# Optimization experiments

Measured on AMD Instinct MI355X. Metric: run time of the kernel, lower is better.

Reference implementation:

```python
import jax, jax.numpy as jnp
import numpy as np

# 2nd-order Sobel kernels (kornia get_sobel_kernel2d_2nd_order): d2/dx2, d2/dxdy, d2/dy2
_KXX = np.array([[1., -2., 1.], [2., -4., 2.], [1., -2., 1.]], np.float32)
_KXY = np.array([[-1., 0., 1.], [0., 0., 0.], [1., 0., -1.]], np.float32)
_KERNELS = jnp.asarray(np.stack([_KXX, _KXY, _KXX.T])[:, None])  # (3,1,3,3)


def setup_inputs() -> dict:
    key = jax.random.key(0)
    x = jax.random.normal(key, (16, 3, 1024, 1024), dtype=jnp.float32)
    return {"x": x}


def reference(x):
    scale = 1.0
    B, C, H, W = x.shape
    # spatial_gradient_2nd_order: replicate pad + 3x3 conv per channel
    xp = jnp.pad(x.reshape(B * C, 1, H, W), ((0, 0), (0, 0), (1, 1), (1, 1)), mode='edge')
    g = jax.lax.conv_general_dilated(xp, _KERNELS, (1, 1), 'VALID')  # (B*C, 3, H, W)
    gxx, gxy, gyy = g[:, 0], g[:, 1], g[:, 2]
    # abs determinant of Hessian, clamp
    scores = jnp.abs(gxx * gyy - gxy * gxy) * (scale ** 4)
    scores = jnp.maximum(scores, 1e-6).reshape(B, C, H, W)
    # NMS via 3x3 max-pool (stride 1, SAME): keep only local maxima
    pooled = jax.lax.reduce_window(scores, -jnp.inf, jax.lax.max,
                                   (1, 1, 3, 3), (1, 1, 1, 1), 'SAME')
    scores = jnp.where(scores == pooled, scores, jnp.zeros((), scores.dtype))
    # global max normalization (adaptive_max_pool2d to 1x1)
    smax = jnp.max(scores, axis=(2, 3), keepdims=True)  # (B,C,1,1)
    return scores / smax
```

## Files before the change

### kernel.cpp

```cpp
#include <hip/hip_runtime.h>

#define H 1024
#define W 1024
#define HW (H * W)
#define STRIP 32
#define SLOTF 1024
#define RING 6

typedef __attribute__((address_space(3))) float lds_f;
typedef const __attribute__((address_space(1))) float g_f;
typedef float nfloat4 __attribute__((ext_vector_type(4)));

__device__ __forceinline__ void gload16(const float* g, float* l) {
    __builtin_amdgcn_global_load_lds((g_f*)g, (lds_f*)l, 16, 0, 0);
}

template<int N>
__device__ __forceinline__ void wait_vm_barrier() {
    asm volatile("s_waitcnt vmcnt(%0)\n\ts_barrier" :: "i"(N) : "memory");
}
__device__ __forceinline__ void barrier_only() {
    asm volatile("s_barrier" ::: "memory");
}

__device__ __forceinline__ void stage(const float* px, int row, float* slotbase, int wq, int t) {
    row = row < 0 ? 0 : (row > H - 1 ? H - 1 : row);
    gload16(px + (size_t)row * W + (t << 2), slotbase + wq);
}

__device__ __forceinline__ float score_ref(
    float a00, float a01, float a02,
    float a10, float a11, float a12,
    float a20, float a21, float a22)
{
#pragma clang fp contract(off)
    float gxx = fmaf(-2.0f, a01, a00);
    gxx = gxx + a02;
    gxx = fmaf(2.0f, a10, gxx);
    gxx = fmaf(-4.0f, a11, gxx);
    gxx = fmaf(2.0f, a12, gxx);
    gxx = gxx + a20;
    gxx = fmaf(-2.0f, a21, gxx);
    gxx = gxx + a22;
    float gxy = a02 - a00;
    gxy = gxy + a20;
    gxy = gxy - a22;
    float gyy = fmaf(2.0f, a01, a00);
    gyy = gyy + a02;
    gyy = fmaf(-2.0f, a10, gyy);
    gyy = fmaf(-4.0f, a11, gyy);
    gyy = fmaf(-2.0f, a12, gyy);
    gyy = gyy + a20;
    gyy = fmaf(2.0f, a21, gyy);
    gyy = gyy + a22;

    float p1 = gxx * gyy;
    float p2 = gxy * gxy;
    float det = p1 - p2;
    float s = fabsf(det);
    return s > 1e-6f ? s : 1e-6f;
}

struct Row8 { float a[8]; };

__device__ __forceinline__ Row8 read_win(const float* p, int t)
{
    const int c = t << 2;
    const float2 L  = *(const float2*)(p + (t == 0 ? 0 : c - 2));
    const float4 M  = *(const float4*)(p + c);
    const float2 Rr = *(const float2*)(p + (t == 255 ? 1022 : c + 4));
    Row8 r;
    r.a[0] = L.x;
    r.a[1] = (t == 0) ? L.x : L.y;
    r.a[2] = M.x; r.a[3] = M.y; r.a[4] = M.z; r.a[5] = M.w;
    r.a[6] = (t == 255) ? Rr.y : Rr.x;
    r.a[7] = Rr.y;
    return r;
}

__global__ __launch_bounds__(256) void hess_max_kernel(
    const float* __restrict__ x, unsigned int* __restrict__ pmax)
{
    __shared__ float lds[RING * SLOTF];
    const int plane = blockIdx.y;
    const int y0 = blockIdx.x * STRIP;
    const int t = threadIdx.x;
    const int wq = (t >> 6) << 8;
    const float* px = x + (size_t)plane * HW;

#pragma unroll
    for (int k = 0; k < RING; ++k)
        stage(px, y0 - 1 + k, lds + k * SLOTF, wq, t);
    wait_vm_barrier<4>();
    Row8 A = read_win(lds, t);
    Row8 B = read_win(lds + SLOTF, t);
    barrier_only();

    float smax = 1e-6f;
    int si = 0, sr = 2;
    for (int i = 0; i < STRIP; ++i) {
        if (i < STRIP - 4) {
            stage(px, y0 + i + 5, lds + si * SLOTF, wq, t);
            si = si + 1 == RING ? 0 : si + 1;
            wait_vm_barrier<4>();
        } else {
            wait_vm_barrier<0>();
        }
        Row8 C = read_win(lds + sr * SLOTF, t);
        sr = sr + 1 == RING ? 0 : sr + 1;

        float P[6], Q[6], Rv[6];
#pragma unroll
        for (int k = 0; k < 6; ++k) {
            P[k]  = fmaf(2.0f, B.a[k + 1], A.a[k + 1]) + C.a[k + 1];
            Q[k]  = fmaf(-2.0f, B.a[k + 1], A.a[k + 1]) + C.a[k + 1];
            Rv[k] = A.a[k + 1] - C.a[k + 1];
        }
#pragma unroll
        for (int j = 0; j < 4; ++j) {
            float gxx = fmaf(-2.0f, P[j + 1], P[j]) + P[j + 2];
            float gyy = fmaf(2.0f, Q[j + 1], Q[j]) + Q[j + 2];
            float gxy = Rv[j + 2] - Rv[j];
            float det = fmaf(gxx, gyy, -(gxy * gxy));
            smax = fmaxf(smax, fabsf(det));
        }
        A = B; B = C;
    }

#pragma unroll
    for (int off = 32; off > 0; off >>= 1)
        smax = fmaxf(smax, __shfl_down(smax, off));
    if ((t & 63) == 0)
        atomicMax(pmax + plane, __float_as_uint(smax));
}

struct S6 { float s[6]; };

__device__ __forceinline__ S6 score_row_exact(const Row8& A, const Row8& B, const Row8& C)
{
    S6 o;
#pragma unroll
    for (int i = 0; i < 6; ++i)
        o.s[i] = score_ref(A.a[i], A.a[i + 1], A.a[i + 2],
                           B.a[i], B.a[i + 1], B.a[i + 2],
                           C.a[i], C.a[i + 1], C.a[i + 2]);
    return o;
}

__global__ __launch_bounds__(256) void hess_nms_kernel(
    const float* __restrict__ x, const unsigned int* __restrict__ pmax,
    float* __restrict__ out)
{
    __shared__ float lds[RING * SLOTF];
    const int plane = blockIdx.y;
    const int y0 = blockIdx.x * STRIP;
    const int t = threadIdx.x;
    const int wq = (t >> 6) << 8;
    const float* px = x + (size_t)plane * HW;
    float* po = out + (size_t)plane * HW;
    const float inv = 1.0f / __uint_as_float(pmax[plane]);

#pragma unroll
    for (int k = 0; k < RING; ++k)
        stage(px, y0 - 2 + k, lds + k * SLOTF, wq, t);
    wait_vm_barrier<1>();
    Row8 rm2 = read_win(lds, t);
    Row8 r0  = read_win(lds + SLOTF, t);
    Row8 r1  = read_win(lds + 2 * SLOTF, t);
    Row8 r2  = read_win(lds + 3 * SLOTF, t);
    Row8 r3  = read_win(lds + 4 * SLOTF, t);

    S6 zero;
#pragma unroll
    for (int i = 0; i < 6; ++i) zero.s[i] = 0.0f;

    S6 sp = zero;
    if (y0 > 0) sp = score_row_exact(rm2, r0, r1);
    S6 sc_ = score_row_exact(r0, r1, r2);

    barrier_only();
    stage(px, y0 + 4, lds + 0 * SLOTF, wq, t);
    stage(px, y0 + 5, lds + 1 * SLOTF, wq, t);

    int si = 2, sr = 5;
    for (int i = 0; i < STRIP; ++i) {
        const int sy = y0 + i;
        if (i < STRIP - 3) {
            stage(px, y0 + i + 6, lds + si * SLOTF, wq, t);
            si = si + 1 == RING ? 0 : si + 1;
        }
        if (i == 0)               wait_vm_barrier<3>();
        else if (i == 1)          wait_vm_barrier<4>();
        else if (i == 2)          wait_vm_barrier<5>();
        else if (i < STRIP - 3)   wait_vm_barrier<6>();
        else                      wait_vm_barrier<0>();

        Row8 r4 = read_win(lds + sr * SLOTF, t);
        sr = sr + 1 == RING ? 0 : sr + 1;

        S6 sn = zero;
        if (sy + 1 < H) sn = score_row_exact(r1, r2, r3);

        float m3[6];
#pragma unroll
        for (int k = 0; k < 6; ++k)
            m3[k] = fmaxf(fmaxf(sp.s[k], sc_.s[k]), sn.s[k]);

        nfloat4 o;
#pragma unroll
        for (int j = 0; j < 4; ++j) {
            float s = sc_.s[j + 1];
            float m = fmaxf(fmaxf(m3[j], m3[j + 1]), m3[j + 2]);
            o[j] = (s == m) ? s * inv : 0.0f;
        }
        __builtin_nontemporal_store(o, (nfloat4*)(po + (size_t)sy * W + (t << 2)));

        r1 = r2; r2 = r3; r3 = r4;
        sp = sc_; sc_ = sn;
    }
}

extern "C" void kernel_launch(void* const* d_in, const int* in_sizes, int n_in,
                              void* d_out, int out_size, void* d_ws, size_t ws_size,
                              hipStream_t stream) {
    const float* x = (const float*)d_in[0];
    float* out = (float*)d_out;
    unsigned int* pmax = (unsigned int*)d_ws;
    const int planes = in_sizes[0] / HW;

    hipMemsetAsync(pmax, 0, planes * sizeof(unsigned int), stream);

    dim3 grid(H / STRIP, planes);
    hess_max_kernel<<<grid, 256, 0, stream>>>(x, pmax);
    hess_nms_kernel<<<grid, 256, 0, stream>>>(x, pmax, out);
}
```

Before: 407.0 us.

## Fuse score max into NMS kernel and normalize in separate scaling pass

Removes the separate max-only pass over the input. The NMS kernel now computes the per-plane maximum while writing unnormalized suppressed scores, and a new kernel then rescales the output in place. This trades one read of the input for an extra read-modify-write of the output. It also switches output stores from nontemporal to regular, presumably so the rescale pass can hit in cache.

Measured after the change: 435.0 us. 6.9% more time.

```diff
diff --git a/kernel.cpp b/kernel.cpp
--- a/kernel.cpp
+++ b/kernel.cpp
@@ -9,7 +9,6 @@
 
 typedef __attribute__((address_space(3))) float lds_f;
 typedef const __attribute__((address_space(1))) float g_f;
-typedef float nfloat4 __attribute__((ext_vector_type(4)));
 
 __device__ __forceinline__ void gload16(const float* g, float* l) {
     __builtin_amdgcn_global_load_lds((g_f*)g, (lds_f*)l, 16, 0, 0);
@@ -78,62 +77,6 @@
     return r;
 }
 
-__global__ __launch_bounds__(256) void hess_max_kernel(
-    const float* __restrict__ x, unsigned int* __restrict__ pmax)
-{
-    __shared__ float lds[RING * SLOTF];
-    const int plane = blockIdx.y;
-    const int y0 = blockIdx.x * STRIP;
-    const int t = threadIdx.x;
-    const int wq = (t >> 6) << 8;
-    const float* px = x + (size_t)plane * HW;
-
-#pragma unroll
-    for (int k = 0; k < RING; ++k)
-        stage(px, y0 - 1 + k, lds + k * SLOTF, wq, t);
-    wait_vm_barrier<4>();
-    Row8 A = read_win(lds, t);
-    Row8 B = read_win(lds + SLOTF, t);
-    barrier_only();
-
-    float smax = 1e-6f;
-    int si = 0, sr = 2;
-    for (int i = 0; i < STRIP; ++i) {
-        if (i < STRIP - 4) {
-            stage(px, y0 + i + 5, lds + si * SLOTF, wq, t);
-            si = si + 1 == RING ? 0 : si + 1;
-            wait_vm_barrier<4>();
-        } else {
-            wait_vm_barrier<0>();
-        }
-        Row8 C = read_win(lds + sr * SLOTF, t);
-        sr = sr + 1 == RING ? 0 : sr + 1;
-
-        float P[6], Q[6], Rv[6];
-#pragma unroll
-        for (int k = 0; k < 6; ++k) {
-            P[k]  = fmaf(2.0f, B.a[k + 1], A.a[k + 1]) + C.a[k + 1];
-            Q[k]  = fmaf(-2.0f, B.a[k + 1], A.a[k + 1]) + C.a[k + 1];
-            Rv[k] = A.a[k + 1] - C.a[k + 1];
-        }
-#pragma unroll
-        for (int j = 0; j < 4; ++j) {
-            float gxx = fmaf(-2.0f, P[j + 1], P[j]) + P[j + 2];
-            float gyy = fmaf(2.0f, Q[j + 1], Q[j]) + Q[j + 2];
-            float gxy = Rv[j + 2] - Rv[j];
-            float det = fmaf(gxx, gyy, -(gxy * gxy));
-            smax = fmaxf(smax, fabsf(det));
-        }
-        A = B; B = C;
-    }
-
-#pragma unroll
-    for (int off = 32; off > 0; off >>= 1)
-        smax = fmaxf(smax, __shfl_down(smax, off));
-    if ((t & 63) == 0)
-        atomicMax(pmax + plane, __float_as_uint(smax));
-}
-
 struct S6 { float s[6]; };
 
 __device__ __forceinline__ S6 score_row_exact(const Row8& A, const Row8& B, const Row8& C)
@@ -147,9 +90,9 @@
     return o;
 }
 
-__global__ __launch_bounds__(256) void hess_nms_kernel(
-    const float* __restrict__ x, const unsigned int* __restrict__ pmax,
-    float* __restrict__ out)
+__global__ __launch_bounds__(256, 4) void hess_score_nms(
+    const float* __restrict__ x, float* __restrict__ out,
+    unsigned int* __restrict__ pmax)
 {
     __shared__ float lds[RING * SLOTF];
     const int plane = blockIdx.y;
@@ -158,7 +101,6 @@
     const int wq = (t >> 6) << 8;
     const float* px = x + (size_t)plane * HW;
     float* po = out + (size_t)plane * HW;
-    const float inv = 1.0f / __uint_as_float(pmax[plane]);
 
 #pragma unroll
     for (int k = 0; k < RING; ++k)
@@ -182,6 +124,7 @@
     stage(px, y0 + 4, lds + 0 * SLOTF, wq, t);
     stage(px, y0 + 5, lds + 1 * SLOTF, wq, t);
 
+    float smax = 1e-6f;
     int si = 2, sr = 5;
     for (int i = 0; i < STRIP; ++i) {
         const int sy = y0 + i;
@@ -206,17 +149,40 @@
         for (int k = 0; k < 6; ++k)
             m3[k] = fmaxf(fmaxf(sp.s[k], sc_.s[k]), sn.s[k]);
 
-        nfloat4 o;
+        float4 o;
+        float* ov = (float*)&o;
 #pragma unroll
         for (int j = 0; j < 4; ++j) {
             float s = sc_.s[j + 1];
+            smax = fmaxf(smax, s);
             float m = fmaxf(fmaxf(m3[j], m3[j + 1]), m3[j + 2]);
-            o[j] = (s == m) ? s * inv : 0.0f;
+            ov[j] = (s == m) ? s : 0.0f;
         }
-        __builtin_nontemporal_store(o, (nfloat4*)(po + (size_t)sy * W + (t << 2)));
+        *(float4*)(po + (size_t)sy * W + (t << 2)) = o;
 
         r1 = r2; r2 = r3; r3 = r4;
         sp = sc_; sc_ = sn;
+    }
+
+#pragma unroll
+    for (int off = 32; off > 0; off >>= 1)
+        smax = fmaxf(smax, __shfl_down(smax, off));
+    if ((t & 63) == 0)
+        atomicMax(pmax + plane, __float_as_uint(smax));
+}
+
+__global__ __launch_bounds__(256) void hess_scale(
+    float* __restrict__ out, const unsigned int* __restrict__ pmax)
+{
+    const int plane = blockIdx.y;
+    const float inv = 1.0f / __uint_as_float(pmax[plane]);
+    float4* p = (float4*)(out + (size_t)plane * HW);
+    const int idx = blockIdx.x * 256 + threadIdx.x;
+#pragma unroll
+    for (int k = 0; k < 4; ++k) {
+        float4 v = p[idx + (k << 16)];
+        v.x *= inv; v.y *= inv; v.z *= inv; v.w *= inv;
+        p[idx + (k << 16)] = v;
     }
 }
 
@@ -230,7 +196,9 @@
 
     hipMemsetAsync(pmax, 0, planes * sizeof(unsigned int), stream);
 
-    dim3 grid(H / STRIP, planes);
-    hess_max_kernel<<<grid, 256, 0, stream>>>(x, pmax);
-    hess_nms_kernel<<<grid, 256, 0, stream>>>(x, pmax, out);
-}
+    dim3 grid1(H / STRIP, planes);
+    hess_score_nms<<<grid1, 256, 0, stream>>>(x, out, pmax);
+
+    dim3 grid2(256, planes);
+    hess_scale<<<grid2, 256, 0, stream>>>(out, pmax);
+}
```
